# Kernel tuning notes

Hardware: AMD Instinct MI355X
Metric: run time of the kernel (lower is better)

Reference implementation:

```python
import jax, jax.numpy as jnp
import numpy as np

VOCAB, EMB = 32000, 1024
HID, NLAYERS = 1024, 2
T, B, S = 64, 128, 128


def setup_inputs() -> dict:
    key = jax.random.key(0)
    ks = jax.random.split(key, 16)
    s = 1.0 / np.sqrt(HID)
    inp = {
        "input": jax.random.randint(ks[0], (T, B), 0, VOCAB),
        "h": jax.random.normal(ks[1], (NLAYERS, B, HID), jnp.float32),
        "H": jax.random.normal(ks[2], (S, B, HID), jnp.float32),
        "emb": jax.random.normal(ks[3], (VOCAB, EMB), jnp.float32) * 0.02,
        "w_ih": jax.random.uniform(ks[4], (NLAYERS, 3 * HID, EMB), jnp.float32, -s, s),
        "w_hh": jax.random.uniform(ks[5], (NLAYERS, 3 * HID, HID), jnp.float32, -s, s),
        "b_ih": jax.random.uniform(ks[6], (NLAYERS, 3 * HID), jnp.float32, -s, s),
        "b_hh": jax.random.uniform(ks[7], (NLAYERS, 3 * HID), jnp.float32, -s, s),
        "L1": jax.random.uniform(ks[8], (HID, HID), jnp.float32, -s, s),
        "L2": jax.random.uniform(ks[9], (HID, 2 * HID), jnp.float32, -s, s),
    }
    return inp


def _gru_cell(x, hprev, w_ih, w_hh, b_ih, b_hh):
    # x: (B, in), hprev: (B, HID); torch GRUCell gate order: r, z, n
    gi = x @ w_ih.T + b_ih          # (B, 3H)
    gh = hprev @ w_hh.T + b_hh      # (B, 3H)
    i_r, i_z, i_n = jnp.split(gi, 3, axis=-1)
    h_r, h_z, h_n = jnp.split(gh, 3, axis=-1)
    r = jax.nn.sigmoid(i_r + h_r)
    z = jax.nn.sigmoid(i_z + h_z)
    n = jnp.tanh(i_n + r * h_n)
    return (1.0 - z) * n + z * hprev


def reference(input, h, H, emb, w_ih, w_hh, b_ih, b_hh, L1, L2):
    embed = emb[input]                  # (T, B, EMB)
    Hc = jnp.transpose(H, (1, 0, 2))    # (B, S, HID)

    def step(hcarry, e):
        # stacked GRU cells
        hs = []
        o = e
        for i in range(NLAYERS):
            hi = _gru_cell(o, hcarry[i], w_ih[i], w_hh[i], b_ih[i], b_hh[i])
            hs.append(hi)
            o = hi
        hn = jnp.stack(hs)              # (L, B, HID)
        # global attention
        q1 = o @ L1.T                   # (B, HID)
        a = jax.nn.softmax(jnp.einsum('bsh,bh->bs', Hc, q1), axis=1)
        c = jnp.einsum('bs,bsh->bh', a, Hc)
        out = jnp.tanh(jnp.concatenate([c, o], axis=1) @ L2.T)
        return hn, out

    h_final, output = jax.lax.scan(step, h, embed)
    return output, h_final
```

## Files before the change

### kernel.cpp

```cpp
#include <hip/hip_runtime.h>

#define T_STEPS 64
#define BATCH   128
#define HID     1024
#define H3      3072
#define EMBD    1024
#define SLEN    128
#define BH      (BATCH * HID)

typedef __attribute__((ext_vector_type(8))) short short8;
typedef __attribute__((ext_vector_type(4))) float f32x4;

__device__ __forceinline__ unsigned short f2bf(float x) {
    unsigned int u = __float_as_uint(x);
    unsigned int r = (u + 0x7fffu + ((u >> 16) & 1u)) >> 16;
    return (unsigned short)r;
}
__device__ __forceinline__ float bf2f(unsigned short h) {
    return __uint_as_float(((unsigned int)h) << 16);
}
__device__ __forceinline__ unsigned int pk(unsigned short a, unsigned short b) {
    return (unsigned int)a | ((unsigned int)b << 16);
}
__device__ __forceinline__ void cvt8(const float4& x, const float4& y,
                                     uint4& H, uint4& L) {
    unsigned short h0 = f2bf(x.x), h1 = f2bf(x.y), h2 = f2bf(x.z), h3 = f2bf(x.w);
    unsigned short h4 = f2bf(y.x), h5 = f2bf(y.y), h6 = f2bf(y.z), h7 = f2bf(y.w);
    unsigned short l0 = f2bf(x.x - bf2f(h0)), l1 = f2bf(x.y - bf2f(h1));
    unsigned short l2 = f2bf(x.z - bf2f(h2)), l3 = f2bf(x.w - bf2f(h3));
    unsigned short l4 = f2bf(y.x - bf2f(h4)), l5 = f2bf(y.y - bf2f(h5));
    unsigned short l6 = f2bf(y.z - bf2f(h6)), l7 = f2bf(y.w - bf2f(h7));
    H = make_uint4(pk(h0,h1), pk(h2,h3), pk(h4,h5), pk(h6,h7));
    L = make_uint4(pk(l0,l1), pk(l2,l3), pk(l4,l5), pk(l6,l7));
}
__device__ __forceinline__ float sigf(float x) {
    return 1.f / (1.f + __expf(-x));
}

#define MF(A, B, ACC) ACC = __builtin_amdgcn_mfma_f32_16x16x32_bf16(A, B, ACC, 0, 0, 0)
#define TRI(AH, AL, WH, WL, ACC)  MF(AH, WL, ACC); MF(AL, WH, ACC); MF(AH, WH, ACC);

__global__ __launch_bounds__(256) void conv_planes_k(
    const float* __restrict__ src, short* __restrict__ hi, short* __restrict__ lo)
{
    const long i8 = (long)blockIdx.x * 256 + threadIdx.x;
    float4 x = ((const float4*)src)[i8 * 2];
    float4 y = ((const float4*)src)[i8 * 2 + 1];
    uint4 H, L; cvt8(x, y, H, L);
    ((uint4*)hi)[i8] = H; ((uint4*)lo)[i8] = L;
}

__global__ __launch_bounds__(256) void conv_gather_k(
    const float* __restrict__ emb, const int* __restrict__ input,
    short* __restrict__ hi, short* __restrict__ lo)
{
    const long i8 = (long)blockIdx.x * 256 + threadIdx.x;
    const int c8 = (int)(i8 & 127);
    const long row = i8 >> 7;
    const float* s = emb + (size_t)input[row] * 1024 + c8 * 8;
    float4 x = ((const float4*)s)[0];
    float4 y = ((const float4*)s)[1];
    uint4 H, L; cvt8(x, y, H, L);
    ((uint4*)hi)[i8] = H; ((uint4*)lo)[i8] = L;
}

template<int MODE, bool CONCAT, bool WLO>
__global__ __launch_bounds__(256, 2) void gemm_big(
    const short* __restrict__ A1h, const short* __restrict__ A1l,
    const short* __restrict__ A2h, const short* __restrict__ A2l,
    const short* __restrict__ Wh,  const short* __restrict__ Wl,
    int K, int nn,
    const float* __restrict__ bias,
    float* __restrict__ outf, short* __restrict__ outh, short* __restrict__ outl,
    int ldo)
{
    extern __shared__ short sm[];
    short* Asm = sm;
    short* Wsm = sm + 16384;
    const int tid = threadIdx.x;
    const int wv = tid >> 6, l = tid & 63;
    const int mq = wv >> 1, nq = wv & 1;
    const int gl = l >> 4, r16 = l & 15;

    const int cpx = gridDim.x >> 3;
    const int id = blockIdx.x;
    const int swz = (id & 7) * cpx + (id >> 3);
    const int bm = swz / nn, bn = swz % nn;
    const long Rbase = (long)bm * 128;
    const int  Cbase = bn * 128;

    const int lda = CONCAT ? (K >> 1) : K;
    const int NC = K >> 5;
    const int NCh = NC >> 1;

    const short *aP1[4], *aP2[4], *wP[4];
    int slda[4];
    #pragma unroll
    for (int j = 0; j < 4; ++j) {
        const int s = tid + j * 256;
        const int pl = s >> 9, sp = s & 511;
        const int row = ((sp >> 6) << 4) | (sp & 15);
        const int kg = (sp >> 4) & 3;
        slda[j] = s * 8;
        const short* a1 = pl ? A1l : A1h;
        aP1[j] = a1 + (Rbase + row) * (long)lda + kg * 8;
        if (CONCAT) {
            const short* a2 = pl ? A2l : A2h;
            aP2[j] = a2 + (Rbase + row) * (long)lda + kg * 8;
        } else aP2[j] = aP1[j];
        const short* wp = pl ? Wl : Wh;
        wP[j] = wp + ((long)Cbase + row) * (long)K + kg * 8;
    }

    f32x4 acc[4][4];
    #pragma unroll
    for (int i = 0; i < 4; ++i)
        #pragma unroll
        for (int j = 0; j < 4; ++j) acc[i][j] = (f32x4)0.f;

    short8 rA[4], rW[4];
    auto LOADC = [&](int c) {
        const bool p1 = !CONCAT || (c < NCh);
        const long ko = p1 ? (long)c * 32 : (long)c * 32 - (K >> 1);
        #pragma unroll
        for (int j = 0; j < 4; ++j) {
            rA[j] = *(const short8*)((p1 ? aP1[j] : aP2[j]) + ko);
            rW[j] = *(const short8*)(wP[j] + (long)c * 32);
        }
    };
    auto STORE = [&](int c) {
        const int b = (c & 1) << 13;
        #pragma unroll
        for (int j = 0; j < 4; ++j) {
            *(short8*)(Asm + b + slda[j]) = rA[j];
            *(short8*)(Wsm + b + slda[j]) = rW[j];
        }
    };

    LOADC(0); STORE(0); LOADC(1);
    __syncthreads();

    for (int c = 0; c < NC; ++c) {
        const int b = (c & 1) << 13;
        short8 ah[4], al[4], wh[4], wl[4];
        #pragma unroll
        for (int f = 0; f < 4; ++f) {
            const short* ab = Asm + b + ((mq * 4 + f) * 64 + l) * 8;
            ah[f] = *(const short8*)ab;
            al[f] = *(const short8*)(ab + 4096);
            const short* wb = Wsm + b + ((nq * 4 + f) * 64 + l) * 8;
            wh[f] = *(const short8*)wb;
            if (!WLO) wl[f] = *(const short8*)(wb + 4096);
        }
        if (c + 1 < NC) STORE(c + 1);
        if (c + 2 < NC) LOADC(c + 2);
        #pragma unroll
        for (int mf = 0; mf < 4; ++mf)
            #pragma unroll
            for (int nf = 0; nf < 4; ++nf) {
                if constexpr (WLO) {
                    MF(al[mf], wh[nf], acc[mf][nf]);
                    MF(ah[mf], wh[nf], acc[mf][nf]);
                } else {
                    TRI(ah[mf], al[mf], wh[nf], wl[nf], acc[mf][nf]);
                }
            }
        __syncthreads();
    }

    #pragma unroll
    for (int mf = 0; mf < 4; ++mf) {
        #pragma unroll
        for (int reg = 0; reg < 4; ++reg) {
            const long R = Rbase + mq * 64 + mf * 16 + gl * 4 + reg;
            #pragma unroll
            for (int nf = 0; nf < 4; ++nf) {
                const int col = Cbase + nq * 64 + nf * 16 + r16;
                const float v = acc[mf][nf][reg];
                if constexpr (MODE == 0) {
                    outf[R * (long)ldo + col] = v + bias[col];
                } else if constexpr (MODE == 1) {
                    const unsigned short hi = f2bf(v), lo = f2bf(v - bf2f(hi));
                    outh[R * (long)ldo + col] = (short)hi;
                    outl[R * (long)ldo + col] = (short)lo;
                } else {
                    outf[R * (long)ldo + col] = tanhf(v);
                }
            }
        }
    }
}

template<int MODE>
__device__ __forceinline__ void gru_sk(
    short* __restrict__ sm,
    const short* __restrict__ A1h, const short* __restrict__ A1l,
    const short* __restrict__ A2h, const short* __restrict__ A2l,
    const short* __restrict__ W1h, const short* __restrict__ W1l,
    const short* __restrict__ W2h,
    const float* __restrict__ bias1, const float* __restrict__ bias2,
    const float* __restrict__ gi,
    const float* __restrict__ hprev,
    float* __restrict__ outf, short* __restrict__ outh, short* __restrict__ outl)
{
    short* Wb = sm + 16384;
    const int tid = threadIdx.x;
    const int wv = tid >> 6, l = tid & 63;
    const int mt = wv & 1, kp = wv >> 1;
    const int gl = l >> 4, r16 = l & 15;
    const int bm = blockIdx.x, bj = blockIdx.y;
    constexpr int NC = (MODE == 2) ? 8 : 16;

    const short* aP[4]; int aL[4];
    #pragma unroll
    for (int i = 0; i < 4; ++i) {
        const int s = tid + i * 256;
        const int part = s >> 9, pl = (s >> 8) & 1, sl = s & 255;
        const int kc = sl >> 7, m = (sl >> 6) & 1;
        const int g = (kc << 2) | ((sl >> 4) & 3);
        const int row = m * 16 + (sl & 15);
        const short* src = part ? (pl ? A2l : A2h) : (pl ? A1l : A1h);
        aP[i] = src + (size_t)(bm * 32 + row) * HID + g * 8;
        aL[i] = s * 8;
    }
    const short* wP[5]; int wL[5]; bool wV[5];
    #pragma unroll
    for (int i = 0; i < 5; ++i) {
        const int s = tid + i * 256;
        bool v = (s < 1152);
        const int reg3 = s / 384;
        if (MODE == 2 && reg3 == 1) v = false;
        const int sub = s - reg3 * 384;
        const int p = sub >> 7, kc = (sub >> 6) & 1;
        const int g = (kc << 2) | ((sub >> 4) & 3);
        const int jr = sub & 15;
        const short* src = (reg3 == 0) ? W1h : (reg3 == 1) ? W1l : W2h;
        wP[i] = v ? src + (size_t)(p * HID + bj * 16 + jr) * HID + g * 8 : A1h;
        wL[i] = s * 8;
        wV[i] = v;
    }

    f32x4 acc[3];
    acc[0] = (f32x4)0.f; acc[1] = (f32x4)0.f; acc[2] = (f32x4)0.f;

    short8 ra[4], rw[5];
    auto LOADC = [&](int c) {
        #pragma unroll
        for (int i = 0; i < 4; ++i) ra[i] = *(const short8*)(aP[i] + c * 64);
        #pragma unroll
        for (int i = 0; i < 5; ++i)
            if (wV[i]) rw[i] = *(const short8*)(wP[i] + c * 64);
    };
    auto STORE = [&](int c) {
        short* ab = sm + (c & 1) * 8192;
        short* wb = Wb + (c & 1) * 9216;
        #pragma unroll
        for (int i = 0; i < 4; ++i) *(short8*)(ab + aL[i]) = ra[i];
        #pragma unroll
        for (int i = 0; i < 5; ++i)
            if (wV[i]) *(short8*)(wb + wL[i]) = rw[i];
    };

    LOADC(0); STORE(0); LOADC(1);
    __syncthreads();

    for (int c = 0; c < NC; ++c) {
        const short* ab = sm + (c & 1) * 8192 + kp * 4096;
        const short* wb = Wb + (c & 1) * 9216 + kp * 6144;
        short8 fh[2], fl[2], fwh[3][2], fwl[3][2];
        #pragma unroll
        for (int kc = 0; kc < 2; ++kc) {
            const int fo = ((kc * 2 + mt) * 64 + l) * 8;
            fh[kc] = *(const short8*)(ab + fo);
            fl[kc] = *(const short8*)(ab + 2048 + fo);
        }
        #pragma unroll
        for (int p = 0; p < 3; ++p)
            #pragma unroll
            for (int kc = 0; kc < 2; ++kc) {
                const int wo = ((p * 2 + kc) * 64 + l) * 8;
                fwh[p][kc] = *(const short8*)(wb + wo);
                if (MODE == 3 && kp == 0)
                    fwl[p][kc] = *(const short8*)(wb + 3072 + wo);
            }
        if (c + 1 < NC) STORE(c + 1);
        if (c + 2 < NC) LOADC(c + 2);
        #pragma unroll
        for (int p = 0; p < 3; ++p)
            #pragma unroll
            for (int kc = 0; kc < 2; ++kc) {
                if (MODE == 3 && kp == 0) { MF(fh[kc], fwl[p][kc], acc[p]); }
                MF(fl[kc], fwh[p][kc], acc[p]);
                MF(fh[kc], fwh[p][kc], acc[p]);
            }
        __syncthreads();
    }

    float* red = (float*)sm;
    if (kp == 1) {
        #pragma unroll
        for (int p = 0; p < 3; ++p)
            *(f32x4*)(red + ((mt * 3 + p) * 64 + l) * 4) = acc[p];
    }
    __syncthreads();
    if (kp == 1) return;

    f32x4 o0 = *(const f32x4*)(red + ((mt * 3 + 0) * 64 + l) * 4);
    f32x4 o1 = *(const f32x4*)(red + ((mt * 3 + 1) * 64 + l) * 4);
    f32x4 o2 = *(const f32x4*)(red + ((mt * 3 + 2) * 64 + l) * 4);

    const int jc = bj * 16 + r16;
    #pragma unroll
    for (int reg = 0; reg < 4; ++reg) {
        const long R = (long)bm * 32 + mt * 16 + gl * 4 + reg;
        float h;
        if constexpr (MODE == 2) {
            const float* orow = gi + R * H3;
            const float rr = sigf(orow[jc] + acc[0][reg] + o0[reg] + bias1[jc]);
            const float zz = sigf(orow[HID + jc] + acc[1][reg] + o1[reg] + bias1[HID + jc]);
            const float nn = tanhf(orow[2 * HID + jc] +
                                   rr * (acc[2][reg] + o2[reg] + bias1[2 * HID + jc]));
            h = (1.f - zz) * nn + zz * hprev[R * HID + jc];
        } else {
            const float rr = sigf(acc[0][reg] + o0[reg] + bias1[jc] + bias2[jc]);
            const float zz = sigf(acc[1][reg] + o1[reg] + bias1[HID + jc] + bias2[HID + jc]);
            const float nn = tanhf(acc[2][reg] + bias1[2 * HID + jc] +
                                   rr * (o2[reg] + bias2[2 * HID + jc]));
            h = (1.f - zz) * nn + zz * hprev[R * HID + jc];
        }
        outf[R * HID + jc] = h;
        const unsigned short hb = f2bf(h), lb = f2bf(h - bf2f(hb));
        outh[R * HID + jc] = (short)hb;
        outl[R * HID + jc] = (short)lb;
    }
}

struct StepP {
    const short* hih; const short* hil;
    const float* h_in; const float* gi0;
    const short* whh0h;
    const short* wih1h; const short* wih1l; const short* whh1h;
    const float* b_hh0; const float* b_ih1; const float* b_hh1;
    float* h0f; float* h1f;
    short* h0ah; short* h0al; short* h1ah; short* h1al;
};

__global__ __launch_bounds__(256) void step_k(int t, StepP P)
{
    __shared__ short sm[34816];
    if (blockIdx.z == 0) {
        if (t >= T_STEPS) return;
        const short* a1h = t ? P.h0ah + (size_t)(t - 1) * BH : P.hih;
        const short* a1l = t ? P.h0al + (size_t)(t - 1) * BH : P.hil;
        gru_sk<2>(sm, a1h, a1l, a1h + 512, a1l + 512,
                  P.whh0h, nullptr, P.whh0h + 512,
                  P.b_hh0, nullptr,
                  P.gi0 + (size_t)t * BATCH * H3,
                  t ? P.h0f + (size_t)((t - 1) & 1) * BH : P.h_in,
                  P.h0f + (size_t)(t & 1) * BH,
                  P.h0ah + (size_t)t * BH, P.h0al + (size_t)t * BH);
    } else {
        if (t < 1) return;
        const int s = t - 1;
        const short* a2h = s ? P.h1ah + (size_t)(s - 1) * BH : P.hih + BH;
        const short* a2l = s ? P.h1al + (size_t)(s - 1) * BH : P.hil + BH;
        gru_sk<3>(sm, P.h0ah + (size_t)s * BH, P.h0al + (size_t)s * BH, a2h, a2l,
                  P.wih1h, P.wih1l, P.whh1h,
                  P.b_ih1, P.b_hh1,
                  nullptr,
                  s ? P.h1f + (size_t)((s - 1) & 1) * BH : P.h_in + BH,
                  P.h1f + (size_t)(s & 1) * BH,
                  P.h1ah + (size_t)s * BH, P.h1al + (size_t)s * BH);
    }
}

__global__ __launch_bounds__(256) void scores_k(
    const short* __restrict__ Qh, const short* __restrict__ Ql,
    const short* __restrict__ Hh, const short* __restrict__ Hl,
    float* __restrict__ Pall)
{
    extern __shared__ short sm[];
    short* Asm = sm;
    short* Wsm = sm + 8192;
    const int b = blockIdx.x, tid = threadIdx.x;
    const int wv = tid >> 6, l = tid & 63;
    const int gl = l >> 4, cc = l & 15;

    const int arow = ((tid >> 6) & 3) * 16 + (tid & 15);
    const int ag   = (tid >> 4) & 3;
    const short* qhp = Qh + ((long)arow * BATCH + b) * HID + ag * 8;
    const short* qlp = Ql + ((long)arow * BATCH + b) * HID + ag * 8;
    const int aLds = tid * 8;

    const short *whp[2], *wlp[2]; int wLds[2];
    #pragma unroll
    for (int i = 0; i < 2; ++i) {
        const int s = tid + i * 256;
        const int srow = ((s >> 6) & 7) * 16 + (s & 15);
        const int sg   = (s >> 4) & 3;
        whp[i] = Hh + ((long)srow * BATCH + b) * HID + sg * 8;
        wlp[i] = Hl + ((long)srow * BATCH + b) * HID + sg * 8;
        wLds[i] = s * 8;
    }

    f32x4 acc[8];
    #pragma unroll
    for (int i = 0; i < 8; ++i) acc[i] = (f32x4)0.f;

    short8 rAh, rAl, rWh[2], rWl[2];
    auto LOADC = [&](int c) {
        rAh = *(const short8*)(qhp + c * 32);
        rAl = *(const short8*)(qlp + c * 32);
        #pragma unroll
        for (int i = 0; i < 2; ++i) {
            rWh[i] = *(const short8*)(whp[i] + c * 32);
            rWl[i] = *(const short8*)(wlp[i] + c * 32);
        }
    };
    auto STORE = [&](int c) {
        const int bb = c & 1;
        *(short8*)(Asm + bb * 4096 + aLds) = rAh;
        *(short8*)(Asm + bb * 4096 + 2048 + aLds) = rAl;
        #pragma unroll
        for (int i = 0; i < 2; ++i) {
            *(short8*)(Wsm + bb * 8192 + wLds[i]) = rWh[i];
            *(short8*)(Wsm + bb * 8192 + 4096 + wLds[i]) = rWl[i];
        }
    };

    LOADC(0); STORE(0); LOADC(1);
    __syncthreads();
    for (int c = 0; c < 32; ++c) {
        const int bb = c & 1;
        const short* abp = Asm + bb * 4096 + (wv * 64 + l) * 8;
        short8 ah = *(const short8*)abp;
        short8 al = *(const short8*)(abp + 2048);
        if (c + 1 < 32) STORE(c + 1);
        if (c + 2 < 32) LOADC(c + 2);
        #pragma unroll
        for (int jt = 0; jt < 8; ++jt) {
            const short* wbp = Wsm + bb * 8192 + (jt * 64 + l) * 8;
            short8 wh = *(const short8*)wbp;
            short8 wl = *(const short8*)(wbp + 4096);
            TRI(ah, al, wh, wl, acc[jt]);
        }
        __syncthreads();
    }

    #pragma unroll
    for (int reg = 0; reg < 4; ++reg) {
        float m = acc[0][reg];
        #pragma unroll
        for (int jt = 1; jt < 8; ++jt) m = fmaxf(m, acc[jt][reg]);
        #pragma unroll
        for (int off = 1; off < 16; off <<= 1) m = fmaxf(m, __shfl_xor(m, off));
        float e[8], ssum = 0.f;
        #pragma unroll
        for (int jt = 0; jt < 8; ++jt) { e[jt] = __expf(acc[jt][reg] - m); ssum += e[jt]; }
        #pragma unroll
        for (int off = 1; off < 16; off <<= 1) ssum += __shfl_xor(ssum, off);
        const float inv = 1.f / ssum;
        const int t = wv * 16 + gl * 4 + reg;
        #pragma unroll
        for (int jt = 0; jt < 8; ++jt)
            Pall[((long)t * BATCH + b) * SLEN + jt * 16 + cc] = e[jt] * inv;
    }
}

__global__ __launch_bounds__(256) void ctx_k(
    const float* __restrict__ Pall, const float* __restrict__ H,
    short* __restrict__ Ch, short* __restrict__ Cl)
{
    __shared__ float Ps[T_STEPS * SLEN];
    const int b = blockIdx.x, ht = blockIdx.y, tid = threadIdx.x;
    for (int i = 0; i < 32; ++i) {
        const int idx = i * 256 + tid;
        const int t = idx >> 7, s = idx & 127;
        Ps[idx] = Pall[((long)t * BATCH + b) * SLEN + s];
    }
    __syncthreads();
    const int col = ht * 256 + tid;
    for (int tg = 0; tg < 4; ++tg) {
        float a[16];
        #pragma unroll
        for (int j = 0; j < 16; ++j) a[j] = 0.f;
        for (int s = 0; s < SLEN; ++s) {
            const float hv = H[((long)s * BATCH + b) * HID + col];
            #pragma unroll
            for (int j = 0; j < 16; ++j)
                a[j] = fmaf(Ps[(tg * 16 + j) * SLEN + s], hv, a[j]);
        }
        #pragma unroll
        for (int j = 0; j < 16; ++j) {
            const long row = (long)(tg * 16 + j) * BATCH + b;
            const unsigned short hi = f2bf(a[j]);
            const unsigned short lo = f2bf(a[j] - bf2f(hi));
            Ch[row * HID + col] = (short)hi;
            Cl[row * HID + col] = (short)lo;
        }
    }
}

extern "C" void kernel_launch(void* const* d_in, const int* in_sizes, int n_in,
                              void* d_out, int out_size, void* d_ws, size_t ws_size,
                              hipStream_t stream)
{
    const int*   input = (const int*)  d_in[0];
    const float* h_in  = (const float*)d_in[1];
    const float* Hbuf  = (const float*)d_in[2];
    const float* emb   = (const float*)d_in[3];
    const float* w_ih  = (const float*)d_in[4];
    const float* w_hh  = (const float*)d_in[5];
    const float* b_ih  = (const float*)d_in[6];
    const float* b_hh  = (const float*)d_in[7];
    const float* L1    = (const float*)d_in[8];
    const float* L2    = (const float*)d_in[9];

    float* out = (float*)d_out;

    char* basep = (char*)d_ws;
    size_t off = 0;
    auto alloc = [&](size_t bytes) -> char* {
        off = (off + 255) & ~(size_t)255;
        char* p = basep + off; off += bytes; return p;
    };
    short* wihH = (short*)alloc(2L*3072*1024*2); short* wihL = (short*)alloc(2L*3072*1024*2);
    short* whhH = (short*)alloc(2L*3072*1024*2); short* whhL = (short*)alloc(2L*3072*1024*2);
    short* l1h  = (short*)alloc(1024L*1024*2);   short* l1l  = (short*)alloc(1024L*1024*2);
    short* l2h  = (short*)alloc(1024L*2048*2);   short* l2l  = (short*)alloc(1024L*2048*2);
    short* Hh   = (short*)alloc(16777216L*2);    short* Hl   = (short*)alloc(16777216L*2);
    short* hih  = (short*)alloc(262144L*2);      short* hil  = (short*)alloc(262144L*2);
    short* h0ah = (short*)alloc(8388608L*2);     short* h0al = (short*)alloc(8388608L*2);
    short* h1ah = (short*)alloc(8388608L*2);     short* h1al = (short*)alloc(8388608L*2);
    short* eqh  = (short*)alloc(8388608L*2);     short* eql  = (short*)alloc(8388608L*2);
    float* gi0  = (float*)alloc(25165824L*4);
    float* h0f  = (float*)alloc(524288L*4);
    float* h1f  = (float*)alloc(524288L*4);
    float* Pall = (float*)alloc(1048576L*4);
    short* ctxh = (short*)gi0;
    short* ctxl = ctxh + 8388608L;

    const short* wih0h = wihH;
    const short* wih0l = wihL;
    const short* wih1h = wihH + 3145728L;
    const short* wih1l = wihL + 3145728L;
    const short* whh0h = whhH;
    const short* whh1h = whhH + 3145728L;

    const dim3 blk(256);
    const size_t SMB = 32768 * sizeof(short);

    conv_planes_k<<<3072, blk, 0, stream>>>(w_ih, wihH, wihL);
    conv_planes_k<<<3072, blk, 0, stream>>>(w_hh, whhH, whhL);
    conv_planes_k<<<512,  blk, 0, stream>>>(L1, l1h, l1l);
    conv_planes_k<<<1024, blk, 0, stream>>>(L2, l2h, l2l);
    conv_planes_k<<<8192, blk, 0, stream>>>(Hbuf, Hh, Hl);
    conv_planes_k<<<128,  blk, 0, stream>>>(h_in, hih, hil);
    conv_gather_k<<<4096, blk, 0, stream>>>(emb, input, eqh, eql);

    gemm_big<0, false, true><<<dim3(1536), blk, SMB, stream>>>(
        eqh, eql, nullptr, nullptr, wih0h, wih0l, 1024, 24,
        b_ih, gi0, nullptr, nullptr, H3);

    StepP sp;
    sp.hih = hih; sp.hil = hil; sp.h_in = h_in; sp.gi0 = gi0;
    sp.whh0h = whh0h;
    sp.wih1h = wih1h; sp.wih1l = wih1l; sp.whh1h = whh1h;
    sp.b_hh0 = b_hh; sp.b_ih1 = b_ih + H3; sp.b_hh1 = b_hh + H3;
    sp.h0f = h0f; sp.h1f = h1f;
    sp.h0ah = h0ah; sp.h0al = h0al; sp.h1ah = h1ah; sp.h1al = h1al;
    for (int t = 0; t <= T_STEPS; ++t)
        step_k<<<dim3(4, 64, 2), blk, 0, stream>>>(t, sp);

    gemm_big<1, false, false><<<dim3(512), blk, SMB, stream>>>(
        h1ah, h1al, nullptr, nullptr, l1h, l1l, 1024, 8,
        nullptr, nullptr, eqh, eql, HID);
    scores_k<<<dim3(BATCH), blk, 49152, stream>>>(eqh, eql, Hh, Hl, Pall);
    ctx_k<<<dim3(BATCH, 4), blk, 0, stream>>>(Pall, Hbuf, ctxh, ctxl);
    gemm_big<2, true, false><<<dim3(512), blk, SMB, stream>>>(
        ctxh, ctxl, h1ah, h1al, l2h, l2l, 2048, 8,
        nullptr, out, nullptr, nullptr, HID);

    hipMemcpyAsync(out + (long)T_STEPS * BH, h0f + BH, (size_t)BH * 4,
                   hipMemcpyDeviceToDevice, stream);
    hipMemcpyAsync(out + (long)T_STEPS * BH + BH, h1f + BH, (size_t)BH * 4,
                   hipMemcpyDeviceToDevice, stream);
}
```

Measured before the change: 2.329 ms.

## Pre-swizzle recurrent weights and states into MFMA fragment layout, drop LDS staging

```diff
diff --git a/kernel.cpp b/kernel.cpp
--- a/kernel.cpp
+++ b/kernel.cpp
@@ -36,6 +36,13 @@
 __device__ __forceinline__ float sigf(float x) {
     return 1.f / (1.f + __expf(-x));
 }
+__device__ __forceinline__ short8 ldg8(const short* p) {
+    return *(const short8*)p;
+}
+__device__ __forceinline__ size_t flidx(int r, int k) {
+    return ((size_t)((r >> 4) * 32 + (k >> 5)) << 9)
+         + ((((k >> 3) & 3) * 16 + (r & 15)) << 3) + (k & 7);
+}
 
 #define MF(A, B, ACC) ACC = __builtin_amdgcn_mfma_f32_16x16x32_bf16(A, B, ACC, 0, 0, 0)
 #define TRI(AH, AL, WH, WL, ACC)  MF(AH, WL, ACC); MF(AL, WH, ACC); MF(AH, WH, ACC);
@@ -62,6 +69,40 @@
     float4 y = ((const float4*)s)[1];
     uint4 H, L; cvt8(x, y, H, L);
     ((uint4*)hi)[i8] = H; ((uint4*)lo)[i8] = L;
+}
+
+template<bool LO>
+__global__ __launch_bounds__(256) void conv_fl_w(
+    const float* __restrict__ src, short* __restrict__ hi, short* __restrict__ lo)
+{
+    const long g = (long)blockIdx.x * 256 + threadIdx.x;
+    const int col = (int)(g >> 7);
+    const int kb = (int)(g & 127) * 8;
+    const float* s = src + (size_t)col * 1024 + kb;
+    float4 x = ((const float4*)s)[0];
+    float4 y = ((const float4*)s)[1];
+    uint4 H, L; cvt8(x, y, H, L);
+    const size_t fi = (((size_t)(col >> 4) * 32 + (kb >> 5)) << 9)
+                    + ((((kb >> 3) & 3) * 16 + (col & 15)) << 3);
+    *(uint4*)(hi + fi) = H;
+    if (LO) *(uint4*)(lo + fi) = L;
+}
+
+__global__ __launch_bounds__(256) void conv_fl_h(
+    const float* __restrict__ src, short* __restrict__ hi, short* __restrict__ lo)
+{
+    const long g = (long)blockIdx.x * 256 + threadIdx.x;
+    const int row = (int)(g >> 7);
+    const int kb = (int)(g & 127) * 8;
+    const int lay = row >> 7, r = row & 127;
+    const float* s = src + (size_t)row * 1024 + kb;
+    float4 x = ((const float4*)s)[0];
+    float4 y = ((const float4*)s)[1];
+    uint4 H, L; cvt8(x, y, H, L);
+    const size_t fi = (size_t)lay * BH + (((size_t)(r >> 4) * 32 + (kb >> 5)) << 9)
+                    + ((((kb >> 3) & 3) * 16 + (r & 15)) << 3);
+    *(uint4*)(hi + fi) = H;
+    *(uint4*)(lo + fi) = L;
 }
 
 template<int MODE, bool CONCAT, bool WLO>
@@ -176,10 +217,11 @@
             #pragma unroll
             for (int nf = 0; nf < 4; ++nf) {
                 const int col = Cbase + nq * 64 + nf * 16 + r16;
-                const float v = acc[mf][nf][reg];
+                float v = acc[mf][nf][reg];
                 if constexpr (MODE == 0) {
                     outf[R * (long)ldo + col] = v + bias[col];
                 } else if constexpr (MODE == 1) {
+                    if (bias) v += bias[col];
                     const unsigned short hi = f2bf(v), lo = f2bf(v - bf2f(hi));
                     outh[R * (long)ldo + col] = (short)hi;
                     outl[R * (long)ldo + col] = (short)lo;
@@ -191,186 +233,126 @@
     }
 }
 
-template<int MODE>
-__device__ __forceinline__ void gru_sk(
-    short* __restrict__ sm,
-    const short* __restrict__ A1h, const short* __restrict__ A1l,
-    const short* __restrict__ A2h, const short* __restrict__ A2l,
-    const short* __restrict__ W1h, const short* __restrict__ W1l,
-    const short* __restrict__ W2h,
-    const float* __restrict__ bias1, const float* __restrict__ bias2,
-    const float* __restrict__ gi,
-    const float* __restrict__ hprev,
-    float* __restrict__ outf, short* __restrict__ outh, short* __restrict__ outl)
-{
-    short* Wb = sm + 16384;
+struct SP2 {
+    const short *hihF, *hilF;
+    const float* h_in;
+    const short *gih, *gil;
+    const short *whh0F, *wih1Fh, *wih1Fl, *whh1F;
+    const float *b_hh0, *b_ih1, *b_hh1;
+    float *h0f, *h1f;
+    short *h0Fh, *h0Fl, *h1Fh, *h1Fl, *h1ah, *h1al;
+};
+
+__global__ __launch_bounds__(256) void step2_k(int t, SP2 P)
+{
     const int tid = threadIdx.x;
-    const int wv = tid >> 6, l = tid & 63;
-    const int mt = wv & 1, kp = wv >> 1;
-    const int gl = l >> 4, r16 = l & 15;
-    const int bm = blockIdx.x, bj = blockIdx.y;
-    constexpr int NC = (MODE == 2) ? 8 : 16;
-
-    const short* aP[4]; int aL[4];
-    #pragma unroll
-    for (int i = 0; i < 4; ++i) {
-        const int s = tid + i * 256;
-        const int part = s >> 9, pl = (s >> 8) & 1, sl = s & 255;
-        const int kc = sl >> 7, m = (sl >> 6) & 1;
-        const int g = (kc << 2) | ((sl >> 4) & 3);
-        const int row = m * 16 + (sl & 15);
-        const short* src = part ? (pl ? A2l : A2h) : (pl ? A1l : A1h);
-        aP[i] = src + (size_t)(bm * 32 + row) * HID + g * 8;
-        aL[i] = s * 8;
-    }
-    const short* wP[5]; int wL[5]; bool wV[5];
-    #pragma unroll
-    for (int i = 0; i < 5; ++i) {
-        const int s = tid + i * 256;
-        bool v = (s < 1152);
-        const int reg3 = s / 384;
-        if (MODE == 2 && reg3 == 1) v = false;
-        const int sub = s - reg3 * 384;
-        const int p = sub >> 7, kc = (sub >> 6) & 1;
-        const int g = (kc << 2) | ((sub >> 4) & 3);
-        const int jr = sub & 15;
-        const short* src = (reg3 == 0) ? W1h : (reg3 == 1) ? W1l : W2h;
-        wP[i] = v ? src + (size_t)(p * HID + bj * 16 + jr) * HID + g * 8 : A1h;
-        wL[i] = s * 8;
-        wV[i] = v;
-    }
-
-    f32x4 acc[3];
-    acc[0] = (f32x4)0.f; acc[1] = (f32x4)0.f; acc[2] = (f32x4)0.f;
-
-    short8 ra[4], rw[5];
-    auto LOADC = [&](int c) {
-        #pragma unroll
-        for (int i = 0; i < 4; ++i) ra[i] = *(const short8*)(aP[i] + c * 64);
-        #pragma unroll
-        for (int i = 0; i < 5; ++i)
-            if (wV[i]) rw[i] = *(const short8*)(wP[i] + c * 64);
-    };
-    auto STORE = [&](int c) {
-        short* ab = sm + (c & 1) * 8192;
-        short* wb = Wb + (c & 1) * 9216;
-        #pragma unroll
-        for (int i = 0; i < 4; ++i) *(short8*)(ab + aL[i]) = ra[i];
-        #pragma unroll
-        for (int i = 0; i < 5; ++i)
-            if (wV[i]) *(short8*)(wb + wL[i]) = rw[i];
-    };
-
-    LOADC(0); STORE(0); LOADC(1);
-    __syncthreads();
-
-    for (int c = 0; c < NC; ++c) {
-        const short* ab = sm + (c & 1) * 8192 + kp * 4096;
-        const short* wb = Wb + (c & 1) * 9216 + kp * 6144;
-        short8 fh[2], fl[2], fwh[3][2], fwl[3][2];
-        #pragma unroll
-        for (int kc = 0; kc < 2; ++kc) {
-            const int fo = ((kc * 2 + mt) * 64 + l) * 8;
-            fh[kc] = *(const short8*)(ab + fo);
-            fl[kc] = *(const short8*)(ab + 2048 + fo);
-        }
-        #pragma unroll
-        for (int p = 0; p < 3; ++p)
+    const int w = tid >> 6, l = tid & 63;
+    const int gw = blockIdx.x * 4 + w;
+    const int z = gw >> 9;
+    const int r = gw & 511;
+    const int cs = r >> 3, mt = r & 7;
+    const int gl = l >> 4, c16 = l & 15;
+    const int jc = cs * 16 + c16;
+    const size_t aOff = ((size_t)mt * 32 * 64 + l) * 8;
+
+    if (z == 0) {
+        if (t >= T_STEPS) return;
+        const short* Ah = t ? P.h0Fh + (size_t)(t - 1) * BH : P.hihF;
+        const short* Al = t ? P.h0Fl + (size_t)(t - 1) * BH : P.hilF;
+        f32x4 a0 = (f32x4)0.f, a1 = (f32x4)0.f, a2 = (f32x4)0.f;
+        #pragma unroll
+        for (int c = 0; c < 32; ++c) {
+            short8 ah = ldg8(Ah + aOff + c * 512);
+            short8 al = ldg8(Al + aOff + c * 512);
             #pragma unroll
-            for (int kc = 0; kc < 2; ++kc) {
-                const int wo = ((p * 2 + kc) * 64 + l) * 8;
-                fwh[p][kc] = *(const short8*)(wb + wo);
-                if (MODE == 3 && kp == 0)
-                    fwl[p][kc] = *(const short8*)(wb + 3072 + wo);
+            for (int p = 0; p < 3; ++p) {
+                const size_t wi = (((size_t)(p * 64 + cs) * 32 + c) << 9) + l * 8;
+                short8 wh = ldg8(P.whh0F + wi);
+                if (p == 0)      { MF(al, wh, a0); MF(ah, wh, a0); }
+                else if (p == 1) { MF(al, wh, a1); MF(ah, wh, a1); }
+                else             { MF(al, wh, a2); MF(ah, wh, a2); }
             }
-        if (c + 1 < NC) STORE(c + 1);
-        if (c + 2 < NC) LOADC(c + 2);
-        #pragma unroll
-        for (int p = 0; p < 3; ++p)
+        }
+        const float b_r = P.b_hh0[jc], b_z = P.b_hh0[HID + jc], b_n = P.b_hh0[2 * HID + jc];
+        const float* hp = t ? P.h0f + (size_t)((t - 1) & 1) * BH : P.h_in;
+        float* ho = P.h0f + (size_t)(t & 1) * BH;
+        short* oh = P.h0Fh + (size_t)t * BH;
+        short* ol = P.h0Fl + (size_t)t * BH;
+        #pragma unroll
+        for (int reg = 0; reg < 4; ++reg) {
+            const int R = mt * 16 + gl * 4 + reg;
+            const size_t gR = ((size_t)t * 128 + R) * H3;
+            const float gr = bf2f((unsigned short)P.gih[gR + jc]) + bf2f((unsigned short)P.gil[gR + jc]);
+            const float gz = bf2f((unsigned short)P.gih[gR + HID + jc]) + bf2f((unsigned short)P.gil[gR + HID + jc]);
+            const float gn = bf2f((unsigned short)P.gih[gR + 2 * HID + jc]) + bf2f((unsigned short)P.gil[gR + 2 * HID + jc]);
+            const float rr = sigf(gr + a0[reg] + b_r);
+            const float zz = sigf(gz + a1[reg] + b_z);
+            const float nn = tanhf(gn + rr * (a2[reg] + b_n));
+            const float h = (1.f - zz) * nn + zz * hp[(size_t)R * HID + jc];
+            ho[(size_t)R * HID + jc] = h;
+            const unsigned short hb = f2bf(h), lb = f2bf(h - bf2f(hb));
+            const size_t fi = flidx(R, jc);
+            oh[fi] = (short)hb; ol[fi] = (short)lb;
+        }
+    } else {
+        const int s = t - 1;
+        if (s < 0) return;
+        const short* A1h = P.h0Fh + (size_t)s * BH;
+        const short* A1l = P.h0Fl + (size_t)s * BH;
+        const short* A2h = s ? P.h1Fh + (size_t)(s - 1) * BH : P.hihF + BH;
+        const short* A2l = s ? P.h1Fl + (size_t)(s - 1) * BH : P.hilF + BH;
+        f32x4 a0 = (f32x4)0.f, a1 = (f32x4)0.f, a2 = (f32x4)0.f, a3 = (f32x4)0.f;
+        #pragma unroll
+        for (int c = 0; c < 32; ++c) {
+            short8 ah = ldg8(A1h + aOff + c * 512);
+            short8 al = ldg8(A1l + aOff + c * 512);
             #pragma unroll
-            for (int kc = 0; kc < 2; ++kc) {
-                if (MODE == 3 && kp == 0) { MF(fh[kc], fwl[p][kc], acc[p]); }
-                MF(fl[kc], fwh[p][kc], acc[p]);
-                MF(fh[kc], fwh[p][kc], acc[p]);
+            for (int p = 0; p < 3; ++p) {
+                const size_t wi = (((size_t)(p * 64 + cs) * 32 + c) << 9) + l * 8;
+                short8 wh = ldg8(P.wih1Fh + wi);
+                short8 wl = ldg8(P.wih1Fl + wi);
+                if (p == 0)      { TRI(ah, al, wh, wl, a0); }
+                else if (p == 1) { TRI(ah, al, wh, wl, a1); }
+                else             { TRI(ah, al, wh, wl, a2); }
             }
-        __syncthreads();
-    }
-
-    float* red = (float*)sm;
-    if (kp == 1) {
-        #pragma unroll
-        for (int p = 0; p < 3; ++p)
-            *(f32x4*)(red + ((mt * 3 + p) * 64 + l) * 4) = acc[p];
-    }
-    __syncthreads();
-    if (kp == 1) return;
-
-    f32x4 o0 = *(const f32x4*)(red + ((mt * 3 + 0) * 64 + l) * 4);
-    f32x4 o1 = *(const f32x4*)(red + ((mt * 3 + 1) * 64 + l) * 4);
-    f32x4 o2 = *(const f32x4*)(red + ((mt * 3 + 2) * 64 + l) * 4);
-
-    const int jc = bj * 16 + r16;
-    #pragma unroll
-    for (int reg = 0; reg < 4; ++reg) {
-        const long R = (long)bm * 32 + mt * 16 + gl * 4 + reg;
-        float h;
-        if constexpr (MODE == 2) {
-            const float* orow = gi + R * H3;
-            const float rr = sigf(orow[jc] + acc[0][reg] + o0[reg] + bias1[jc]);
-            const float zz = sigf(orow[HID + jc] + acc[1][reg] + o1[reg] + bias1[HID + jc]);
-            const float nn = tanhf(orow[2 * HID + jc] +
-                                   rr * (acc[2][reg] + o2[reg] + bias1[2 * HID + jc]));
-            h = (1.f - zz) * nn + zz * hprev[R * HID + jc];
-        } else {
-            const float rr = sigf(acc[0][reg] + o0[reg] + bias1[jc] + bias2[jc]);
-            const float zz = sigf(acc[1][reg] + o1[reg] + bias1[HID + jc] + bias2[HID + jc]);
-            const float nn = tanhf(acc[2][reg] + bias1[2 * HID + jc] +
-                                   rr * (o2[reg] + bias2[2 * HID + jc]));
-            h = (1.f - zz) * nn + zz * hprev[R * HID + jc];
-        }
-        outf[R * HID + jc] = h;
-        const unsigned short hb = f2bf(h), lb = f2bf(h - bf2f(hb));
-        outh[R * HID + jc] = (short)hb;
-        outl[R * HID + jc] = (short)lb;
-    }
-}
-
-struct StepP {
-    const short* hih; const short* hil;
-    const float* h_in; const float* gi0;
-    const short* whh0h;
-    const short* wih1h; const short* wih1l; const short* whh1h;
-    const float* b_hh0; const float* b_ih1; const float* b_hh1;
-    float* h0f; float* h1f;
-    short* h0ah; short* h0al; short* h1ah; short* h1al;
-};
-
-__global__ __launch_bounds__(256) void step_k(int t, StepP P)
-{
-    __shared__ short sm[34816];
-    if (blockIdx.z == 0) {
-        if (t >= T_STEPS) return;
-        const short* a1h = t ? P.h0ah + (size_t)(t - 1) * BH : P.hih;
-        const short* a1l = t ? P.h0al + (size_t)(t - 1) * BH : P.hil;
-        gru_sk<2>(sm, a1h, a1l, a1h + 512, a1l + 512,
-                  P.whh0h, nullptr, P.whh0h + 512,
-                  P.b_hh0, nullptr,
-                  P.gi0 + (size_t)t * BATCH * H3,
-                  t ? P.h0f + (size_t)((t - 1) & 1) * BH : P.h_in,
-                  P.h0f + (size_t)(t & 1) * BH,
-                  P.h0ah + (size_t)t * BH, P.h0al + (size_t)t * BH);
-    } else {
-        if (t < 1) return;
-        const int s = t - 1;
-        const short* a2h = s ? P.h1ah + (size_t)(s - 1) * BH : P.hih + BH;
-        const short* a2l = s ? P.h1al + (size_t)(s - 1) * BH : P.hil + BH;
-        gru_sk<3>(sm, P.h0ah + (size_t)s * BH, P.h0al + (size_t)s * BH, a2h, a2l,
-                  P.wih1h, P.wih1l, P.whh1h,
-                  P.b_ih1, P.b_hh1,
-                  nullptr,
-                  s ? P.h1f + (size_t)((s - 1) & 1) * BH : P.h_in + BH,
-                  P.h1f + (size_t)(s & 1) * BH,
-                  P.h1ah + (size_t)s * BH, P.h1al + (size_t)s * BH);
+        }
+        #pragma unroll
+        for (int c = 0; c < 32; ++c) {
+            short8 ah = ldg8(A2h + aOff + c * 512);
+            short8 al = ldg8(A2l + aOff + c * 512);
+            #pragma unroll
+            for (int p = 0; p < 3; ++p) {
+                const size_t wi = (((size_t)(p * 64 + cs) * 32 + c) << 9) + l * 8;
+                short8 wh = ldg8(P.whh1F + wi);
+                if (p == 0)      { MF(al, wh, a0); MF(ah, wh, a0); }
+                else if (p == 1) { MF(al, wh, a1); MF(ah, wh, a1); }
+                else             { MF(al, wh, a3); MF(ah, wh, a3); }
+            }
+        }
+        const float bir = P.b_ih1[jc] + P.b_hh1[jc];
+        const float biz = P.b_ih1[HID + jc] + P.b_hh1[HID + jc];
+        const float bin = P.b_ih1[2 * HID + jc];
+        const float bhn = P.b_hh1[2 * HID + jc];
+        const float* hp = s ? P.h1f + (size_t)((s - 1) & 1) * BH : P.h_in + BH;
+        float* ho = P.h1f + (size_t)(s & 1) * BH;
+        short* oh = P.h1Fh + (size_t)s * BH;
+        short* ol = P.h1Fl + (size_t)s * BH;
+        short* rh = P.h1ah + (size_t)s * BH;
+        short* rl = P.h1al + (size_t)s * BH;
+        #pragma unroll
+        for (int reg = 0; reg < 4; ++reg) {
+            const int R = mt * 16 + gl * 4 + reg;
+            const float rr = sigf(a0[reg] + bir);
+            const float zz = sigf(a1[reg] + biz);
+            const float nn = tanhf(a2[reg] + bin + rr * (a3[reg] + bhn));
+            const float h = (1.f - zz) * nn + zz * hp[(size_t)R * HID + jc];
+            ho[(size_t)R * HID + jc] = h;
+            const unsigned short hb = f2bf(h), lb = f2bf(h - bf2f(hb));
+            const size_t fi = flidx(R, jc);
+            oh[fi] = (short)hb; ol[fi] = (short)lb;
+            rh[(size_t)R * HID + jc] = (short)hb;
+            rl[(size_t)R * HID + jc] = (short)lb;
+        }
     }
 }
 
@@ -524,53 +506,52 @@
         off = (off + 255) & ~(size_t)255;
         char* p = basep + off; off += bytes; return p;
     };
-    short* wihH = (short*)alloc(2L*3072*1024*2); short* wihL = (short*)alloc(2L*3072*1024*2);
-    short* whhH = (short*)alloc(2L*3072*1024*2); short* whhL = (short*)alloc(2L*3072*1024*2);
-    short* l1h  = (short*)alloc(1024L*1024*2);   short* l1l  = (short*)alloc(1024L*1024*2);
-    short* l2h  = (short*)alloc(1024L*2048*2);   short* l2l  = (short*)alloc(1024L*2048*2);
-    short* Hh   = (short*)alloc(16777216L*2);    short* Hl   = (short*)alloc(16777216L*2);
-    short* hih  = (short*)alloc(262144L*2);      short* hil  = (short*)alloc(262144L*2);
-    short* h0ah = (short*)alloc(8388608L*2);     short* h0al = (short*)alloc(8388608L*2);
-    short* h1ah = (short*)alloc(8388608L*2);     short* h1al = (short*)alloc(8388608L*2);
-    short* eqh  = (short*)alloc(8388608L*2);     short* eql  = (short*)alloc(8388608L*2);
-    float* gi0  = (float*)alloc(25165824L*4);
-    float* h0f  = (float*)alloc(524288L*4);
-    float* h1f  = (float*)alloc(524288L*4);
-    float* Pall = (float*)alloc(1048576L*4);
-    short* ctxh = (short*)gi0;
-    short* ctxl = ctxh + 8388608L;
-
-    const short* wih0h = wihH;
-    const short* wih0l = wihL;
-    const short* wih1h = wihH + 3145728L;
-    const short* wih1l = wihL + 3145728L;
-    const short* whh0h = whhH;
-    const short* whh1h = whhH + 3145728L;
+    short* wih0h = (short*)alloc(3145728L*2); short* wih0l = (short*)alloc(3145728L*2);
+    short* l1h   = (short*)alloc(1048576L*2); short* l1l   = (short*)alloc(1048576L*2);
+    short* l2h   = (short*)alloc(2097152L*2); short* l2l   = (short*)alloc(2097152L*2);
+    short* Hh    = (short*)alloc(16777216L*2); short* Hl   = (short*)alloc(16777216L*2);
+    short* hihF  = (short*)alloc(262144L*2);  short* hilF  = (short*)alloc(262144L*2);
+    short* h0Fh  = (short*)alloc(8388608L*2); short* h0Fl  = (short*)alloc(8388608L*2);
+    short* h1Fh  = (short*)alloc(8388608L*2); short* h1Fl  = (short*)alloc(8388608L*2);
+    short* h1ah  = (short*)alloc(8388608L*2); short* h1al  = (short*)alloc(8388608L*2);
+    short* eqh   = (short*)alloc(8388608L*2); short* eql   = (short*)alloc(8388608L*2);
+    short* gi0h  = (short*)alloc(25165824L*2); short* gi0l = (short*)alloc(25165824L*2);
+    short* whh0F = (short*)alloc(3145728L*2);
+    short* wih1Fh= (short*)alloc(3145728L*2); short* wih1Fl= (short*)alloc(3145728L*2);
+    short* whh1F = (short*)alloc(3145728L*2);
+    float* h0f   = (float*)alloc(524288L*4);
+    float* h1f   = (float*)alloc(524288L*4);
+    float* Pall  = (float*)alloc(1048576L*4);
+    short* ctxh  = gi0h;
+    short* ctxl  = gi0h + 8388608L;
 
     const dim3 blk(256);
     const size_t SMB = 32768 * sizeof(short);
 
-    conv_planes_k<<<3072, blk, 0, stream>>>(w_ih, wihH, wihL);
-    conv_planes_k<<<3072, blk, 0, stream>>>(w_hh, whhH, whhL);
+    conv_planes_k<<<1536, blk, 0, stream>>>(w_ih, wih0h, wih0l);
     conv_planes_k<<<512,  blk, 0, stream>>>(L1, l1h, l1l);
     conv_planes_k<<<1024, blk, 0, stream>>>(L2, l2h, l2l);
     conv_planes_k<<<8192, blk, 0, stream>>>(Hbuf, Hh, Hl);
-    conv_planes_k<<<128,  blk, 0, stream>>>(h_in, hih, hil);
     conv_gather_k<<<4096, blk, 0, stream>>>(emb, input, eqh, eql);
-
-    gemm_big<0, false, true><<<dim3(1536), blk, SMB, stream>>>(
+    conv_fl_h<<<128, blk, 0, stream>>>(h_in, hihF, hilF);
+    conv_fl_w<false><<<1536, blk, 0, stream>>>(w_hh, whh0F, nullptr);
+    conv_fl_w<true><<<1536, blk, 0, stream>>>(w_ih + 3145728L, wih1Fh, wih1Fl);
+    conv_fl_w<false><<<1536, blk, 0, stream>>>(w_hh + 3145728L, whh1F, nullptr);
+
+    gemm_big<1, false, true><<<dim3(1536), blk, SMB, stream>>>(
         eqh, eql, nullptr, nullptr, wih0h, wih0l, 1024, 24,
-        b_ih, gi0, nullptr, nullptr, H3);
-
-    StepP sp;
-    sp.hih = hih; sp.hil = hil; sp.h_in = h_in; sp.gi0 = gi0;
-    sp.whh0h = whh0h;
-    sp.wih1h = wih1h; sp.wih1l = wih1l; sp.whh1h = whh1h;
+        b_ih, nullptr, gi0h, gi0l, H3);
+
+    SP2 sp;
+    sp.hihF = hihF; sp.hilF = hilF; sp.h_in = h_in;
+    sp.gih = gi0h; sp.gil = gi0l;
+    sp.whh0F = whh0F; sp.wih1Fh = wih1Fh; sp.wih1Fl = wih1Fl; sp.whh1F = whh1F;
     sp.b_hh0 = b_hh; sp.b_ih1 = b_ih + H3; sp.b_hh1 = b_hh + H3;
     sp.h0f = h0f; sp.h1f = h1f;
-    sp.h0ah = h0ah; sp.h0al = h0al; sp.h1ah = h1ah; sp.h1al = h1al;
+    sp.h0Fh = h0Fh; sp.h0Fl = h0Fl; sp.h1Fh = h1Fh; sp.h1Fl = h1Fl;
+    sp.h1ah = h1ah; sp.h1al = h1al;
     for (int t = 0; t <= T_STEPS; ++t)
-        step_k<<<dim3(4, 64, 2), blk, 0, stream>>>(t, sp);
+        step2_k<<<dim3(256), blk, 0, stream>>>(t, sp);
 
     gemm_big<1, false, false><<<dim3(512), blk, SMB, stream>>>(
         h1ah, h1al, nullptr, nullptr, l1h, l1l, 1024, 8,
```

Result: slower. 3.706 ms (+59.1%).
